# Optimization experiments

Hardware: AMD Instinct MI355X
Metric: run time of the kernel (lower is better)

Reference implementation:

```python
import jax, jax.numpy as jnp
import numpy as np

B, T, F = 256, 2048, 20
H_NODES = 256


def _heaviside(x):
    # smooth heaviside approx used throughout the original module
    return (jnp.tanh(10.0 * x) + 1.0) * 0.5


def _evap(wu, wl, wd, pet):
    h = _heaviside
    et1 = h(wu - pet) * pet + h(pet - wu) * wu
    rp = h(pet - et1) * (pet - et1)  # h(-(pet-et1))*0 term vanishes
    et22 = h(rp - wl) * wl + h(wl - rp) * rp
    et2 = h(rp) * et22
    et33 = h(rp - et2 - wd) * wd + h(wd - (rp - et2)) * (rp - et2)
    et3 = h(rp - et2) * et33
    return et1, et2, et3


def _runoff(wu, wl, wd, p, wum, wlm, wdm, b, c):
    wum = wum * 19.9 + 0.1
    wlm = wlm * 30.0 + 60.0
    wdm = wdm * 60.0 + 60.0
    c = c * 0.19 + 0.01
    b = b * 0.3 + 0.1
    w_total = wum + wlm + wdm
    s = c * (wu / w_total) ** 2 + b * (wl / w_total) ** 2
    return _heaviside(p - s) * (p - s)


def _partition(runoff, k1, k2, k3):
    k1 = k1 * 0.69 + 0.01
    k2 = k2 * 0.69 + 0.01
    k3 = k3 * 0.89 + 0.01
    sr = k1 * runoff
    itf = k2 * (runoff - sr)
    bf = k3 * (runoff - sr - itf)
    return sr, itf, bf


def setup_inputs() -> dict:
    key = jax.random.key(0)
    ks = jax.random.split(key, 7)
    u = lambda k, shp: jax.random.uniform(k, shp, jnp.float32, -0.05, 0.05)
    inputs = jax.random.uniform(ks[0], (B, T, F), jnp.float32)
    return {
        "inputs": inputs,
        "w1": u(ks[1], (15, H_NODES)),
        "b1": jnp.zeros((H_NODES,), jnp.float32),
        "w2": u(ks[2], (H_NODES, 64)),
        "b2": jnp.zeros((64,), jnp.float32),
        "w3": u(ks[3], (64, 8)),
        "b3": jnp.zeros((8,), jnp.float32),
    }


def reference(inputs, w1, b1, w2, b2, w3, b3):
    pet = inputs[..., 0:1]
    tmean = inputs[..., 1:2]
    p = inputs[..., 2:3]
    attrs = inputs[..., 5:]  # [B,T,15]

    # static-attribute -> physical-parameter MLP
    h1 = jnp.tanh(attrs @ w1 + b1)
    h2 = jnp.tanh(h1 @ w2 + b2)
    params = jax.nn.sigmoid(h2 @ w3 + b3)  # [B,T,8]

    xs = jnp.concatenate([pet, p, tmean, params], axis=-1)  # [B,T,11]

    def step(state, x):
        wu, wl, wd = state[:, 0:1], state[:, 1:2], state[:, 2:3]
        pet_t, p_t = x[:, 0:1], x[:, 1:2]
        et1, et2, et3 = _evap(wu, wl, wd, pet_t)
        clip = lambda d: jnp.clip(d, -1e5, 1e5)
        wu_n = wu + clip(p_t - et1)
        wl_n = wl + clip(p_t - et1 - et2)
        wd_n = wd + clip(p_t - et1 - et2 - et3)
        ns = jnp.concatenate([wu_n, wl_n, wd_n], axis=1)  # [B,3]
        return ns, ns

    init = jnp.zeros((inputs.shape[0], 3), inputs.dtype)
    _, outs = jax.lax.scan(step, init, jnp.swapaxes(xs, 0, 1))  # [T,B,3]
    outputs = jnp.swapaxes(outs, 0, 1)  # [B,T,3]

    wu, wl, wd = outputs[..., 0:1], outputs[..., 1:2], outputs[..., 2:3]
    wum, wlm, wdm = params[..., 0:1], params[..., 1:2], params[..., 2:3]
    b, c = params[..., 3:4], params[..., 4:5]
    k1, k2, k3 = params[..., 5:6], params[..., 6:7], params[..., 7:8]

    et1, et2, et3 = _evap(wu, wl, wd, pet)
    # NOTE: original call() swaps (wl,wd) and (wlm,wdm) here - kept faithful
    runoff = _runoff(wu, wd, wl, p, wum, wdm, wlm, b, c)
    sr, itf, bf = _partition(runoff, k1, k2, k3)
    total_q = sr + itf * 0.5 + bf * 0.25  # flow routing
    return total_q  # [B,T,1]
```

## Files before the change

### kernel.cpp

```cpp
#include <hip/hip_runtime.h>

#define B_ 256
#define T_ 2048
#define F_ 20
#define NT (B_*T_)
#define CH 16
#define NCH (T_/CH)

typedef __bf16 bf16x8 __attribute__((ext_vector_type(8)));
typedef float  f32x4  __attribute__((ext_vector_type(4)));

__device__ __forceinline__ float ex2(float x){ return __builtin_amdgcn_exp2f(x); }
__device__ __forceinline__ float rcpf_(float x){ return __builtin_amdgcn_rcpf(x); }

#define K10F 28.853900817779268f
#define INVK 0.034657359027997264f
#define K1F   2.8853900817779268f
#define LOG2E 1.4426950408889634f

__device__ __forceinline__ float hside(float x){ return 1.0f - rcpf_(ex2(K10F*x) + 1.0f); }
__device__ __forceinline__ float tanh_f(float z){ return 1.0f - 2.0f*rcpf_(ex2(K1F*z) + 1.0f); }
__device__ __forceinline__ float sigmoid_f(float z){ return rcpf_(1.0f + ex2(-LOG2E*z)); }


__global__ __launch_bounds__(256) void prep_kernel(const float* __restrict__ in,
                                                   float* __restrict__ ws){
  int r = blockIdx.x*256 + threadIdx.x;
  if (r >= NT) return;
  int b = r & (B_-1);
  int t = r >> 8;
  const float* src = in + ((size_t)b*T_ + t)*F_;
  ((float2*)ws)[r] = make_float2(src[0], src[2]);
}

__global__ __launch_bounds__(512) void fused_kernel(const float* __restrict__ in,
    const float* __restrict__ w1, const float* __restrict__ b1,
    const float* __restrict__ w2, const float* __restrict__ b2,
    const float* __restrict__ w3, const float* __restrict__ b3,
    float* __restrict__ ws){
  extern __shared__ char sm[];
  float* params = ws + 4*(size_t)NT;

  if (blockIdx.x < 8) {
    const float2* pp2 = (const float2*)ws;
    float* wuT = ws + 2*(size_t)NT;
    float* wdT = ws + 3*(size_t)NT;
    float2* ppL = (float2*)sm;
    float2* dkb = (float2*)(sm + 8192);
    float2* rhb = (float2*)(sm + 16384);
    float2* qbb = (float2*)(sm + 24576);
    float*  bb2 = (float*)(sm + 32768);
    float*  wub = (float*)(sm + 36864);
    float*  wdb = (float*)(sm + 40960);

    int tid  = threadIdx.x;
    int wv   = tid >> 6;
    int l64  = tid & 63;
    bool act = l64 < 32;
    int lane = l64 & 31;
    int boff = blockIdx.x * 32;

    float Wu = 0.0f, WL = 0.0f, WD = 0.0f;

    if (wv == 4 && act){
      float2 v[CH];
      #pragma unroll
      for (int s = 0; s < CH; ++s) v[s] = pp2[s*B_ + boff + lane];
      #pragma unroll
      for (int s = 0; s < CH; ++s)
        ppL[s*32 + lane] = make_float2(K10F*v[s].x, K10F*(v[s].y - v[s].x));
    }
    __syncthreads();

    for (int it = 0; it < NCH + 4; ++it){
      if (wv == 0){
        int c = it;
        if (c < NCH && act){
          int par = c & 1;
          #pragma unroll
          for (int s = 0; s < CH; ++s){
            float2 pe = ppL[(par*CH + s)*32 + lane];
            float t1  = Wu - pe.x;
            float r   = rcpf_(ex2(t1) + 1.0f);
            float WuPP= Wu + pe.y;
            float Wn  = fmaf(-t1, r, WuPP);
            float dK  = -t1*r;
            float BASE= pe.y + dK;
            dkb[(par*CH + s)*32 + lane] = make_float2(dK, BASE);
            wub[(par*CH + s)*32 + lane] = Wn;
            Wu = Wn;
          }
        }
      } else if (wv == 1){
        int c = it - 1;
        if (c >= 0 && c < NCH && act){
          int par = c & 1;
          #pragma unroll
          for (int s = 0; s < CH; ++s){
            float2 db = dkb[(par*CH + s)*32 + lane];
            float r1  = rcpf_(ex2(db.x) + 1.0f);
            float RP  = fmaf(-db.x, r1, db.x);
            float HRP = 1.0f - rcpf_(ex2(RP) + 1.0f);
            rhb[(par*CH + s)*32 + lane] = make_float2(RP, HRP);
            bb2[(par*CH + s)*32 + lane] = db.y;
          }
        }
      } else if (wv == 2){
        int c = it - 2;
        if (c >= 0 && c < NCH && act){
          int par = c & 1;
          #pragma unroll
          for (int s = 0; s < CH; ++s){
            float2 rh  = rhb[(par*CH + s)*32 + lane];
            float BASE = bb2[(par*CH + s)*32 + lane];
            float D2   = rh.x - WL;
            float r    = rcpf_(ex2(D2) + 1.0f);
            float et22 = fmaf(D2, r, WL);
            float WLB  = WL + BASE;
            float Wn   = fmaf(-rh.y, et22, WLB);
            float ET2  = rh.y * et22;
            qbb[(par*CH + s)*32 + lane] = make_float2(rh.x - ET2, BASE - ET2);
            WL = Wn;
          }
        }
      } else if (wv == 3){
        int c = it - 3;
        if (c >= 0 && c < NCH && act){
          int par = c & 1;
          #pragma unroll
          for (int s = 0; s < CH; ++s){
            float2 qb  = qbb[(par*CH + s)*32 + lane];
            float hqv  = 1.0f - rcpf_(ex2(qb.x) + 1.0f);
            float D3   = qb.x - WD;
            float r    = rcpf_(ex2(D3) + 1.0f);
            float et33 = fmaf(D3, r, WD);
            float WDB  = WD + qb.y;
            float Wn   = fmaf(-hqv, et33, WDB);
            wdb[(par*CH + s)*32 + lane] = Wn;
            WD = Wn;
          }
        }
      } else if (wv == 4){
        int cn = it + 1;
        if (cn < NCH && act){
          float2 v[CH];
          #pragma unroll
          for (int s = 0; s < CH; ++s) v[s] = pp2[(cn*CH + s)*B_ + boff + lane];
          int par = cn & 1;
          #pragma unroll
          for (int s = 0; s < CH; ++s)
            ppL[(par*CH + s)*32 + lane] = make_float2(K10F*v[s].x, K10F*(v[s].y - v[s].x));
        }
      } else if (wv == 5){
        int cw = it - 1;
        if (cw >= 0 && cw < NCH && act){
          int par = cw & 1;
          #pragma unroll
          for (int s = 0; s < CH; ++s)
            wuT[(cw*CH + s)*B_ + boff + lane] = wub[(par*CH + s)*32 + lane] * INVK;
        }
        int cd = it - 4;
        if (cd >= 0 && cd < NCH && act){
          int par = cd & 1;
          #pragma unroll
          for (int s = 0; s < CH; ++s)
            wdT[(cd*CH + s)*B_ + boff + lane] = wdb[(par*CH + s)*32 + lane] * INVK;
        }
      }
      __syncthreads();
    }
    return;
  }

  __bf16* w1f  = (__bf16*)sm;
  __bf16* w2f  = (__bf16*)(sm + 8192);
  float*  b1s  = (float*)(sm + 40960);
  float*  b2s  = (float*)(sm + 41984);
  float*  w3s  = (float*)(sm + 42240);
  float*  b3s  = (float*)(sm + 44288);
  __bf16* hbufA= (__bf16*)(sm + 44320);

  int tid = threadIdx.x;

  for (int s = tid; s < 16*32*8; s += 512) w1f[s] = (__bf16)0.0f;
  __syncthreads();
  for (int idx = tid; idx < 15*256; idx += 512){
    int k = idx >> 8, n = idx & 255;
    int ct = n >> 4;
    int l  = ((k>>3)*16) + (n & 15);
    int j  = k & 7;
    w1f[(ct*32 + l)*8 + j] = (__bf16)w1[idx];
  }
  for (int idx = tid; idx < 256*64; idx += 512){
    int k = idx >> 6, n = idx & 63;
    int kb = k >> 5;
    int lq = (k >> 3) & 3;
    int j  = k & 7;
    int ct = n >> 4;
    int l  = lq*16 + (n & 15);
    w2f[((kb*4 + ct)*64 + l)*8 + j] = (__bf16)w2[idx];
  }
  if (tid < 256) b1s[tid] = b1[tid];
  if (tid < 64)  b2s[tid] = b2[tid];
  if (tid < 512) w3s[tid] = w3[tid];
  if (tid < 8)   b3s[tid] = b3[tid];
  __syncthreads();

  int lane = tid & 63;
  int wv   = tid >> 6;
  int m    = lane & 15;
  int q    = lane >> 4;
  int r0   = (blockIdx.x - 8)*128 + wv*16;

  int rowA = r0 + m;
  int bA = rowA & (B_-1), tA = rowA >> 8;
  const float* ap = in + ((size_t)bA*T_ + tA)*F_ + 5;
  bf16x8 a1;
  #pragma unroll
  for (int j = 0; j < 8; ++j){
    int k = q*8 + j;
    float v = (k < 15) ? ap[k] : 0.0f;
    a1[j] = (__bf16)v;
  }

  __bf16* hb = hbufA + wv*1152;
  f32x4 zero4 = {0.0f, 0.0f, 0.0f, 0.0f};
  bf16x8 zero8;
  #pragma unroll
  for (int j = 0; j < 8; ++j) zero8[j] = (__bf16)0.0f;

  f32x4 acc2[4] = {zero4, zero4, zero4, zero4};

  #pragma unroll
  for (int p = 0; p < 4; ++p){
    #pragma unroll
    for (int c4 = 0; c4 < 4; ++c4){
      int ct = p*4 + c4;
      bf16x8 bw = zero8;
      if (lane < 32) bw = *(const bf16x8*)&w1f[(ct*32 + lane)*8];
      f32x4 c1 = __builtin_amdgcn_mfma_f32_16x16x32_bf16(a1, bw, zero4, 0, 0, 0);
      int f = c4*16 + m;
      float bb = b1s[p*64 + f];
      #pragma unroll
      for (int i = 0; i < 4; ++i){
        float h = tanh_f(c1[i] + bb);
        hb[(q*4 + i)*72 + f] = (__bf16)h;
      }
    }
    #pragma unroll
    for (int kb = 0; kb < 2; ++kb){
      bf16x8 a2 = *(const bf16x8*)&hb[m*72 + q*8 + kb*32];
      #pragma unroll
      for (int ct = 0; ct < 4; ++ct){
        bf16x8 bw2 = *(const bf16x8*)&w2f[(((p*2 + kb)*4 + ct)*64 + lane)*8];
        acc2[ct] = __builtin_amdgcn_mfma_f32_16x16x32_bf16(a2, bw2, acc2[ct], 0, 0, 0);
      }
    }
  }

  #pragma unroll
  for (int ct = 0; ct < 4; ++ct){
    int f = ct*16 + m;
    float bb = b2s[f];
    #pragma unroll
    for (int i = 0; i < 4; ++i){
      float h = tanh_f(acc2[ct][i] + bb);
      hb[(q*4 + i)*72 + f] = (__bf16)h;
    }
  }

  float z0 = b3s[2*q], z1 = b3s[2*q + 1];
  #pragma unroll
  for (int kb3 = 0; kb3 < 8; ++kb3){
    bf16x8 hv8 = *(const bf16x8*)&hb[m*72 + kb3*8];
    #pragma unroll
    for (int j = 0; j < 8; ++j){
      float hv = (float)hv8[j];
      int k = kb3*8 + j;
      z0 = fmaf(hv, w3s[k*8 + 2*q],     z0);
      z1 = fmaf(hv, w3s[k*8 + 2*q + 1], z1);
    }
  }
  int rowO = r0 + m;
  float2 outp = make_float2(sigmoid_f(z0), sigmoid_f(z1));
  *(float2*)&params[(size_t)rowO*8 + 2*q] = outp;
}

__global__ __launch_bounds__(256) void final_kernel(const float* __restrict__ ws,
                                                    float* __restrict__ out){
  __shared__ float tile[64*65];
  int tb = blockIdx.x & 31;
  int bb = blockIdx.x >> 5;
  int t0 = tb*64, b0 = bb*64;
  int tid = threadIdx.x;
  const float2* pp2 = (const float2*)ws;
  const float* wuT  = ws + 2*(size_t)NT;
  const float* wdT  = ws + 3*(size_t)NT;
  const float* params = ws + 4*(size_t)NT;

  #pragma unroll
  for (int k = 0; k < 16; ++k){
    int idx = k*256 + tid;
    int tl = idx >> 6, bl = idx & 63;
    int r = (t0 + tl)*B_ + b0 + bl;
    float p  = pp2[r].y;
    float wu = wuT[r], wd = wdT[r];
    const float4* pp = (const float4*)(params + (size_t)r*8);
    float4 p0 = pp[0], p1 = pp[1];
    float wum   = fmaf(p0.x, 19.9f, 0.1f);
    float wlm_s = fmaf(p0.z, 30.0f, 60.0f);
    float wdm_s = fmaf(p0.y, 60.0f, 60.0f);
    float cc = fmaf(p1.x, 0.19f, 0.01f);
    float bcoef = fmaf(p0.w, 0.30f, 0.10f);
    float wt = wum + wlm_s + wdm_s;
    float xu = wu / wt;
    float xd = wd / wt;
    float s  = cc*xu*xu + bcoef*xd*xd;
    float ps = p - s;
    float runoff = hside(ps)*ps;
    float k1p = fmaf(p1.y, 0.69f, 0.01f);
    float k2p = fmaf(p1.z, 0.69f, 0.01f);
    float k3p = fmaf(p1.w, 0.89f, 0.01f);
    float sr  = k1p*runoff;
    float itf = k2p*(runoff - sr);
    float bf  = k3p*(runoff - sr - itf);
    tile[bl*65 + tl] = sr + 0.5f*itf + 0.25f*bf;
  }
  __syncthreads();
  #pragma unroll
  for (int k = 0; k < 16; ++k){
    int idx = k*256 + tid;
    int tl2 = idx & 63, bl2 = idx >> 6;
    out[(size_t)(b0 + bl2)*T_ + t0 + tl2] = tile[bl2*65 + tl2];
  }
}

extern "C" void kernel_launch(void* const* d_in, const int* in_sizes, int n_in,
                              void* d_out, int out_size, void* d_ws, size_t ws_size,
                              hipStream_t stream) {
  const float* in = (const float*)d_in[0];
  const float* w1 = (const float*)d_in[1];
  const float* b1 = (const float*)d_in[2];
  const float* w2 = (const float*)d_in[3];
  const float* b2 = (const float*)d_in[4];
  const float* w3 = (const float*)d_in[5];
  const float* b3 = (const float*)d_in[6];
  float* out = (float*)d_out;
  float* ws  = (float*)d_ws;

  prep_kernel <<<NT/256,      256, 0,     stream>>>(in, ws);
  fused_kernel<<<NT/128 + 8,  512, 62752, stream>>>(in, w1, b1, w2, b2, w3, b3, ws);
  final_kernel<<<128,         256, 0,     stream>>>(ws, out);
}
```

Baseline: 229.7 us.

## Drop prep kernel, use natural b-major layout, deepen scan pipeline buffers

```diff
diff --git a/kernel.cpp b/kernel.cpp
--- a/kernel.cpp
+++ b/kernel.cpp
@@ -23,35 +23,22 @@
 __device__ __forceinline__ float sigmoid_f(float z){ return rcpf_(1.0f + ex2(-LOG2E*z)); }
 
 
-__global__ __launch_bounds__(256) void prep_kernel(const float* __restrict__ in,
-                                                   float* __restrict__ ws){
-  int r = blockIdx.x*256 + threadIdx.x;
-  if (r >= NT) return;
-  int b = r & (B_-1);
-  int t = r >> 8;
-  const float* src = in + ((size_t)b*T_ + t)*F_;
-  ((float2*)ws)[r] = make_float2(src[0], src[2]);
-}
-
-__global__ __launch_bounds__(512) void fused_kernel(const float* __restrict__ in,
+__global__ __launch_bounds__(512, 4) void fused_kernel(const float* __restrict__ in,
     const float* __restrict__ w1, const float* __restrict__ b1,
     const float* __restrict__ w2, const float* __restrict__ b2,
     const float* __restrict__ w3, const float* __restrict__ b3,
     float* __restrict__ ws){
   extern __shared__ char sm[];
-  float* params = ws + 4*(size_t)NT;
+  float* params2 = ws + 2*(size_t)NT;
 
   if (blockIdx.x < 8) {
-    const float2* pp2 = (const float2*)ws;
-    float* wuT = ws + 2*(size_t)NT;
-    float* wdT = ws + 3*(size_t)NT;
+    float2* wwT = (float2*)ws;
     float2* ppL = (float2*)sm;
     float2* dkb = (float2*)(sm + 8192);
-    float2* rhb = (float2*)(sm + 16384);
-    float2* qbb = (float2*)(sm + 24576);
-    float*  bb2 = (float*)(sm + 32768);
-    float*  wub = (float*)(sm + 36864);
-    float*  wdb = (float*)(sm + 40960);
+    float2* rhb = (float2*)(sm + 24576);
+    float2* qbb = (float2*)(sm + 32768);
+    float*  wub = (float*)(sm + 40960);
+    float*  wdb = (float*)(sm + 57344);
 
     int tid  = threadIdx.x;
     int wv   = tid >> 6;
@@ -59,13 +46,17 @@
     bool act = l64 < 32;
     int lane = l64 & 31;
     int boff = blockIdx.x * 32;
+    int bmy  = boff + lane;
 
     float Wu = 0.0f, WL = 0.0f, WD = 0.0f;
 
     if (wv == 4 && act){
-      float2 v[CH];
+    float2 v[CH];
       #pragma unroll
-      for (int s = 0; s < CH; ++s) v[s] = pp2[s*B_ + boff + lane];
+      for (int s = 0; s < CH; ++s){
+        float4 r4 = *(const float4*)(in + ((size_t)bmy*T_ + s)*F_);
+        v[s] = make_float2(r4.x, r4.z);
+      }
       #pragma unroll
       for (int s = 0; s < CH; ++s)
         ppL[s*32 + lane] = make_float2(K10F*v[s].x, K10F*(v[s].y - v[s].x));
@@ -76,50 +67,55 @@
       if (wv == 0){
         int c = it;
         if (c < NCH && act){
-          int par = c & 1;
-          #pragma unroll
-          for (int s = 0; s < CH; ++s){
-            float2 pe = ppL[(par*CH + s)*32 + lane];
-            float t1  = Wu - pe.x;
-            float r   = rcpf_(ex2(t1) + 1.0f);
-            float WuPP= Wu + pe.y;
-            float Wn  = fmaf(-t1, r, WuPP);
-            float dK  = -t1*r;
-            float BASE= pe.y + dK;
-            dkb[(par*CH + s)*32 + lane] = make_float2(dK, BASE);
-            wub[(par*CH + s)*32 + lane] = Wn;
+          int par = c & 1, pd = c & 3, pw = c & 7;
+          float2 pe[CH];
+          #pragma unroll
+          for (int s = 0; s < CH; ++s) pe[s] = ppL[(par*CH + s)*32 + lane];
+          #pragma unroll
+          for (int s = 0; s < CH; ++s){
+            float t1 = Wu - pe[s].x;
+            float r  = rcpf_(ex2(t1) + 1.0f);
+            float dK = -t1*r;
+            float BASE = pe[s].y + dK;
+            float Wn = Wu + BASE;
+            dkb[(pd*CH + s)*32 + lane] = make_float2(dK, BASE);
+            wub[(pw*CH + s)*32 + lane] = Wn;
             Wu = Wn;
           }
         }
       } else if (wv == 1){
         int c = it - 1;
         if (c >= 0 && c < NCH && act){
-          int par = c & 1;
-          #pragma unroll
-          for (int s = 0; s < CH; ++s){
-            float2 db = dkb[(par*CH + s)*32 + lane];
-            float r1  = rcpf_(ex2(db.x) + 1.0f);
-            float RP  = fmaf(-db.x, r1, db.x);
+          int par = c & 1, pd = c & 3;
+          float dk[CH];
+          #pragma unroll
+          for (int s = 0; s < CH; ++s) dk[s] = dkb[(pd*CH + s)*32 + lane].x;
+          #pragma unroll
+          for (int s = 0; s < CH; ++s){
+            float r1  = rcpf_(ex2(dk[s]) + 1.0f);
+            float RP  = fmaf(-dk[s], r1, dk[s]);
             float HRP = 1.0f - rcpf_(ex2(RP) + 1.0f);
             rhb[(par*CH + s)*32 + lane] = make_float2(RP, HRP);
-            bb2[(par*CH + s)*32 + lane] = db.y;
           }
         }
       } else if (wv == 2){
         int c = it - 2;
         if (c >= 0 && c < NCH && act){
-          int par = c & 1;
-          #pragma unroll
-          for (int s = 0; s < CH; ++s){
-            float2 rh  = rhb[(par*CH + s)*32 + lane];
-            float BASE = bb2[(par*CH + s)*32 + lane];
-            float D2   = rh.x - WL;
+          int par = c & 1, pd = c & 3;
+          float2 rh[CH]; float bs[CH];
+          #pragma unroll
+          for (int s = 0; s < CH; ++s) rh[s] = rhb[(par*CH + s)*32 + lane];
+          #pragma unroll
+          for (int s = 0; s < CH; ++s) bs[s] = dkb[(pd*CH + s)*32 + lane].y;
+          #pragma unroll
+          for (int s = 0; s < CH; ++s){
+            float D2   = rh[s].x - WL;
             float r    = rcpf_(ex2(D2) + 1.0f);
             float et22 = fmaf(D2, r, WL);
-            float WLB  = WL + BASE;
-            float Wn   = fmaf(-rh.y, et22, WLB);
-            float ET2  = rh.y * et22;
-            qbb[(par*CH + s)*32 + lane] = make_float2(rh.x - ET2, BASE - ET2);
+            float WLB  = WL + bs[s];
+            float Wn   = fmaf(-rh[s].y, et22, WLB);
+            float ET2  = rh[s].y * et22;
+            qbb[(par*CH + s)*32 + lane] = make_float2(rh[s].x - ET2, bs[s] - ET2);
             WL = Wn;
           }
         }
@@ -127,14 +123,16 @@
         int c = it - 3;
         if (c >= 0 && c < NCH && act){
           int par = c & 1;
-          #pragma unroll
-          for (int s = 0; s < CH; ++s){
-            float2 qb  = qbb[(par*CH + s)*32 + lane];
-            float hqv  = 1.0f - rcpf_(ex2(qb.x) + 1.0f);
-            float D3   = qb.x - WD;
+          float2 qb[CH];
+          #pragma unroll
+          for (int s = 0; s < CH; ++s) qb[s] = qbb[(par*CH + s)*32 + lane];
+          #pragma unroll
+          for (int s = 0; s < CH; ++s){
+            float hqv  = 1.0f - rcpf_(ex2(qb[s].x) + 1.0f);
+            float D3   = qb[s].x - WD;
             float r    = rcpf_(ex2(D3) + 1.0f);
             float et33 = fmaf(D3, r, WD);
-            float WDB  = WD + qb.y;
+            float WDB  = WD + qb[s].y;
             float Wn   = fmaf(-hqv, et33, WDB);
             wdb[(par*CH + s)*32 + lane] = Wn;
             WD = Wn;
@@ -145,26 +143,28 @@
         if (cn < NCH && act){
           float2 v[CH];
           #pragma unroll
-          for (int s = 0; s < CH; ++s) v[s] = pp2[(cn*CH + s)*B_ + boff + lane];
+          for (int s = 0; s < CH; ++s){
+            float4 r4 = *(const float4*)(in + ((size_t)bmy*T_ + cn*CH + s)*F_);
+            v[s] = make_float2(r4.x, r4.z);
+          }
           int par = cn & 1;
           #pragma unroll
           for (int s = 0; s < CH; ++s)
             ppL[(par*CH + s)*32 + lane] = make_float2(K10F*v[s].x, K10F*(v[s].y - v[s].x));
         }
       } else if (wv == 5){
-        int cw = it - 1;
-        if (cw >= 0 && cw < NCH && act){
-          int par = cw & 1;
+        int c = it - 4;
+        if (c >= 0 && c < NCH && act){
+          int pw = c & 7, par = c & 1;
+          float wuv[CH], wdv[CH];
+          #pragma unroll
+          for (int s = 0; s < CH; ++s) wuv[s] = wub[(pw*CH + s)*32 + lane];
+          #pragma unroll
+          for (int s = 0; s < CH; ++s) wdv[s] = wdb[(par*CH + s)*32 + lane];
+          float2* dst = &wwT[(size_t)bmy*T_ + c*CH];
           #pragma unroll
           for (int s = 0; s < CH; ++s)
-            wuT[(cw*CH + s)*B_ + boff + lane] = wub[(par*CH + s)*32 + lane] * INVK;
-        }
-        int cd = it - 4;
-        if (cd >= 0 && cd < NCH && act){
-          int par = cd & 1;
-          #pragma unroll
-          for (int s = 0; s < CH; ++s)
-            wdT[(cd*CH + s)*B_ + boff + lane] = wdb[(par*CH + s)*32 + lane] * INVK;
+            dst[s] = make_float2(wuv[s]*INVK, wdv[s]*INVK);
         }
       }
       __syncthreads();
@@ -212,9 +212,8 @@
   int q    = lane >> 4;
   int r0   = (blockIdx.x - 8)*128 + wv*16;
 
-  int rowA = r0 + m;
-  int bA = rowA & (B_-1), tA = rowA >> 8;
-  const float* ap = in + ((size_t)bA*T_ + tA)*F_ + 5;
+  int rho = r0 + m;
+  const float* ap = in + (size_t)rho*F_ + 5;
   bf16x8 a1;
   #pragma unroll
   for (int j = 0; j < 8; ++j){
@@ -281,58 +280,41 @@
       z1 = fmaf(hv, w3s[k*8 + 2*q + 1], z1);
     }
   }
-  int rowO = r0 + m;
   float2 outp = make_float2(sigmoid_f(z0), sigmoid_f(z1));
-  *(float2*)&params[(size_t)rowO*8 + 2*q] = outp;
+  *(float2*)&params2[(size_t)rho*8 + 2*q] = outp;
 }
 
-__global__ __launch_bounds__(256) void final_kernel(const float* __restrict__ ws,
+__global__ __launch_bounds__(256) void final_kernel(const float* __restrict__ in,
+                                                    const float* __restrict__ ws,
                                                     float* __restrict__ out){
-  __shared__ float tile[64*65];
-  int tb = blockIdx.x & 31;
-  int bb = blockIdx.x >> 5;
-  int t0 = tb*64, b0 = bb*64;
-  int tid = threadIdx.x;
-  const float2* pp2 = (const float2*)ws;
-  const float* wuT  = ws + 2*(size_t)NT;
-  const float* wdT  = ws + 3*(size_t)NT;
-  const float* params = ws + 4*(size_t)NT;
-
-  #pragma unroll
-  for (int k = 0; k < 16; ++k){
-    int idx = k*256 + tid;
-    int tl = idx >> 6, bl = idx & 63;
-    int r = (t0 + tl)*B_ + b0 + bl;
-    float p  = pp2[r].y;
-    float wu = wuT[r], wd = wdT[r];
-    const float4* pp = (const float4*)(params + (size_t)r*8);
-    float4 p0 = pp[0], p1 = pp[1];
-    float wum   = fmaf(p0.x, 19.9f, 0.1f);
-    float wlm_s = fmaf(p0.z, 30.0f, 60.0f);
-    float wdm_s = fmaf(p0.y, 60.0f, 60.0f);
-    float cc = fmaf(p1.x, 0.19f, 0.01f);
-    float bcoef = fmaf(p0.w, 0.30f, 0.10f);
-    float wt = wum + wlm_s + wdm_s;
-    float xu = wu / wt;
-    float xd = wd / wt;
-    float s  = cc*xu*xu + bcoef*xd*xd;
-    float ps = p - s;
-    float runoff = hside(ps)*ps;
-    float k1p = fmaf(p1.y, 0.69f, 0.01f);
-    float k2p = fmaf(p1.z, 0.69f, 0.01f);
-    float k3p = fmaf(p1.w, 0.89f, 0.01f);
-    float sr  = k1p*runoff;
-    float itf = k2p*(runoff - sr);
-    float bf  = k3p*(runoff - sr - itf);
-    tile[bl*65 + tl] = sr + 0.5f*itf + 0.25f*bf;
-  }
-  __syncthreads();
-  #pragma unroll
-  for (int k = 0; k < 16; ++k){
-    int idx = k*256 + tid;
-    int tl2 = idx & 63, bl2 = idx >> 6;
-    out[(size_t)(b0 + bl2)*T_ + t0 + tl2] = tile[bl2*65 + tl2];
-  }
+  int rho = blockIdx.x*256 + threadIdx.x;
+  if (rho >= NT) return;
+  const float2* wwT = (const float2*)ws;
+  const float* params2 = ws + 2*(size_t)NT;
+
+  float p  = in[(size_t)rho*F_ + 2];
+  float2 w = wwT[rho];
+  float wu = w.x, wd = w.y;
+  const float4* pp = (const float4*)(params2 + (size_t)rho*8);
+  float4 p0 = pp[0], p1 = pp[1];
+  float wum   = fmaf(p0.x, 19.9f, 0.1f);
+  float wlm_s = fmaf(p0.z, 30.0f, 60.0f);
+  float wdm_s = fmaf(p0.y, 60.0f, 60.0f);
+  float cc = fmaf(p1.x, 0.19f, 0.01f);
+  float bcoef = fmaf(p0.w, 0.30f, 0.10f);
+  float wt = wum + wlm_s + wdm_s;
+  float xu = wu / wt;
+  float xd = wd / wt;
+  float s  = cc*xu*xu + bcoef*xd*xd;
+  float ps = p - s;
+  float runoff = hside(ps)*ps;
+  float k1p = fmaf(p1.y, 0.69f, 0.01f);
+  float k2p = fmaf(p1.z, 0.69f, 0.01f);
+  float k3p = fmaf(p1.w, 0.89f, 0.01f);
+  float sr  = k1p*runoff;
+  float itf = k2p*(runoff - sr);
+  float bf  = k3p*(runoff - sr - itf);
+  out[rho] = sr + 0.5f*itf + 0.25f*bf;
 }
 
 extern "C" void kernel_launch(void* const* d_in, const int* in_sizes, int n_in,
@@ -348,7 +330,6 @@
   float* out = (float*)d_out;
   float* ws  = (float*)d_ws;
 
-  prep_kernel <<<NT/256,      256, 0,     stream>>>(in, ws);
   fused_kernel<<<NT/128 + 8,  512, 62752, stream>>>(in, w1, b1, w2, b2, w3, b3, ws);
-  final_kernel<<<128,         256, 0,     stream>>>(ws, out);
+  final_kernel<<<NT/256,      256, 0,     stream>>>(in, ws, out);
 }
```

Result: slower. 245.0 us (+6.6%).
